# Optimization experiments

Measured on AMD Instinct MI355X. Metric: run time of the kernel, lower is better.

## Reference

```python
import jax, jax.numpy as jnp
import numpy as np

T = 2048        # tokens
HID = 4096      # hidden_size
H = 32          # num attention heads
KV = 8          # num key/value heads (GQA)
D = HID // H    # head_dim = 128
THETA = 10000.0


def setup_inputs() -> dict:
    key = jax.random.key(0)
    k1, k2, k3 = jax.random.split(key, 3)
    hidden_states = jax.random.normal(k1, (T, HID), jnp.float32)
    positions = jnp.arange(T, dtype=jnp.int32)
    Wqkv = jax.random.normal(k2, ((H + 2 * KV) * D, HID), jnp.float32) * 0.02
    Wo = jax.random.normal(k3, (HID, H * D), jnp.float32) * 0.02
    return {"hidden_states": hidden_states, "positions": positions,
            "Wqkv": Wqkv, "Wo": Wo}


def _rope(positions, x):
    """Neox-style rotary embedding. x: [T, h, D], positions: [T]."""
    half = D // 2
    inv_freq = 1.0 / (THETA ** (jnp.arange(half, dtype=jnp.float32) / half))
    ang = positions.astype(jnp.float32)[:, None] * inv_freq      # [T, half]
    cos = jnp.cos(ang)[:, None, :]                                # [T, 1, half]
    sin = jnp.sin(ang)[:, None, :]
    x1, x2 = x[..., :half], x[..., half:]
    return jnp.concatenate([x1 * cos - x2 * sin, x2 * cos + x1 * sin], axis=-1)


def reference(hidden_states, positions, Wqkv, Wo):
    # fused QKV projection (no bias)
    qkv = hidden_states @ Wqkv.T                                  # [T, (H+2KV)*D]
    q, k, v = jnp.split(qkv, [H * D, H * D + KV * D], axis=1)
    q = q.reshape(T, H, D)
    k = k.reshape(T, KV, D)
    v = v.reshape(T, KV, D)
    # RoPE on q and k
    q = _rope(positions, q)
    k = _rope(positions, k)
    # GQA: expand kv heads to match q heads
    g = H // KV
    k = jnp.repeat(k, g, axis=1)                                  # [T, H, D]
    v = jnp.repeat(v, g, axis=1)
    # causal attention (flash-attention math)
    scores = jnp.einsum('thd,shd->hts', q, k) * (D ** -0.5)       # [H, T, T]
    causal = jnp.tril(jnp.ones((T, T), dtype=bool))
    scores = jnp.where(causal[None], scores, jnp.float32(-1e30))
    probs = jax.nn.softmax(scores, axis=-1)
    attn = jnp.einsum('hts,shd->thd', probs, v).reshape(T, H * D)
    # output projection
    return attn @ Wo.T
```

## Files before the change

### kernel.cpp

```cpp
#include <hip/hip_runtime.h>
#include <stdint.h>

#define T_SEQ 2048
#define HIDDEN 4096
#define NHEAD 32
#define NKV 8
#define HDIM 128
#define QKVN 6144

typedef __bf16 bf16x8 __attribute__((ext_vector_type(8)));
typedef float f32x4 __attribute__((ext_vector_type(4)));
typedef unsigned short u16;
typedef u16 u16x8 __attribute__((ext_vector_type(8)));
typedef u16 u16x4 __attribute__((ext_vector_type(4)));

__device__ __forceinline__ u16 f2bf(float f) {
  uint32_t u = __builtin_bit_cast(uint32_t, f);
  u = (u + 0x7fffu + ((u >> 16) & 1u)) >> 16;
  return (u16)u;
}
__device__ __forceinline__ float bf2f(u16 h) {
  uint32_t u = ((uint32_t)h) << 16;
  return __builtin_bit_cast(float, u);
}

__device__ __forceinline__ void gload16(const void* g, void* l) {
  __builtin_amdgcn_global_load_lds(
      (__attribute__((address_space(1))) void*)(uintptr_t)g,
      (__attribute__((address_space(3))) void*)(uintptr_t)l, 16, 0, 0);
}

__global__ void cvt2_kernel(const float* __restrict__ in1, u16* __restrict__ out1, int n1_4,
                            const float* __restrict__ in2, u16* __restrict__ out2, int n2_4) {
  int base = blockIdx.x * blockDim.x + threadIdx.x;
  int stride = gridDim.x * blockDim.x;
  for (int i = base; i < n1_4; i += stride) {
    float4 v = ((const float4*)in1)[i];
    u16x4 o;
    o.x = f2bf(v.x); o.y = f2bf(v.y); o.z = f2bf(v.z); o.w = f2bf(v.w);
    ((u16x4*)out1)[i] = o;
  }
  for (int i = base; i < n2_4; i += stride) {
    float4 v = ((const float4*)in2)[i];
    u16x4 o;
    o.x = f2bf(v.x); o.y = f2bf(v.y); o.z = f2bf(v.z); o.w = f2bf(v.w);
    ((u16x4*)out2)[i] = o;
  }
}

__global__ void prep_kernel(u16* __restrict__ qkv, const int* __restrict__ pos,
                            u16* __restrict__ vt,
                            const float* __restrict__ wo_in, u16* __restrict__ wo_out,
                            int wo_n4) {
  __shared__ u16 tile[64][64];
  const int bid = blockIdx.x;
  const int tid = threadIdx.x;

  if (bid < 512) {
    const int tb = bid & 31;
    const int yy = bid >> 5;
    const int kvh = yy >> 1;
    const int d0 = (yy & 1) * 64;
    const u16* src = qkv + (size_t)(NHEAD + NKV) * HDIM + kvh * HDIM + d0;
#pragma unroll
    for (int g = 0; g < 2; ++g) {
      int u = g * 256 + tid;
      int t = u >> 3, ds = u & 7;
      u16x8 v = *(const u16x8*)(src + (size_t)(tb * 64 + t) * QKVN + ds * 8);
#pragma unroll
      for (int j = 0; j < 8; ++j) {
        int d = ds * 8 + j;
        tile[d][(((t >> 3) ^ (d & 7)) * 8) + (t & 7)] = v[j];
      }
    }
    __syncthreads();
    u16* dst = vt + ((size_t)kvh * HDIM + d0) * T_SEQ + tb * 64;
#pragma unroll
    for (int g = 0; g < 4; ++g) {
      int u = g * 256 + tid;
      int d = u >> 4, qd = u & 15;
      int a = qd >> 3, gg = (qd >> 1) & 3, b = qd & 1;
      int t0 = 32 * a + 16 * b + 4 * gg;
      u16x4 v = *(const u16x4*)&tile[d][(((t0 >> 3) ^ (d & 7)) * 8) + (t0 & 7)];
      *(u16x4*)(dst + (size_t)d * T_SEQ + qd * 4) = v;
    }
    return;
  }

  const int nb = gridDim.x - 512;
  const int base = (bid - 512) * blockDim.x + tid;
  const int stride = nb * blockDim.x;
  for (int idx = base; idx < T_SEQ * 40 * 64; idx += stride) {
    int i = idx & 63;
    int head = (idx >> 6) % 40;
    int t = idx / (40 * 64);
    int hb = head < NHEAD ? head * HDIM : NHEAD * HDIM + (head - NHEAD) * HDIM;
    float p = (float)pos[t];
    float inv_freq = exp2f(-(float)i * (13.287712379549449f / 64.0f));
    float ang = p * inv_freq;
    float s, c;
    sincosf(ang, &s, &c);
    u16* p1 = qkv + (size_t)t * QKVN + hb + i;
    u16* p2 = p1 + 64;
    float x1 = bf2f(*p1), x2 = bf2f(*p2);
    *p1 = f2bf(x1 * c - x2 * s);
    *p2 = f2bf(x2 * c + x1 * s);
  }
  for (int i = base; i < wo_n4; i += stride) {
    float4 v = ((const float4*)wo_in)[i];
    u16x4 o;
    o.x = f2bf(v.x); o.y = f2bf(v.y); o.z = f2bf(v.z); o.w = f2bf(v.w);
    ((u16x4*)wo_out)[i] = o;
  }
}

__device__ __forceinline__ void storeC(float* p, float v) { *p = v; }
__device__ __forceinline__ void storeC(u16* p, float v) { *p = f2bf(v); }
__device__ __forceinline__ f32x4 mfma16(bf16x8 a, bf16x8 b, f32x4 c) {
  return __builtin_amdgcn_mfma_f32_16x16x32_bf16(a, b, c, 0, 0, 0);
}

__global__ void __launch_bounds__(512, 1)
gemm_qkv(const u16* __restrict__ A, const u16* __restrict__ B,
         u16* __restrict__ C, int M, int N, int K) {
  __shared__ u16 As_[2][128 * 64];
  __shared__ u16 Bs_[2][384 * 64];

  const int tid = threadIdx.x;
  const int lane = tid & 63;
  const int w = tid >> 6;
  const int wr = w >> 2, wc = w & 3;
  const int l15 = lane & 15, lg = lane >> 4;

  const int c8 = blockIdx.x & 7, i8 = blockIdx.x >> 3;
  const int by = i8 & 15;
  const int bx = c8 * 2 + (i8 >> 4);
  const int bm = by * 128, bn = bx * 384;

  const int u_lo = w * 64 + lane, u_hi = u_lo + 512;
  const int r0 = u_lo >> 3, s0 = (u_lo & 7) ^ (r0 & 7);
  const int r1 = u_hi >> 3, s1 = (u_hi & 7) ^ (r1 & 7);
  const u16* a_s0 = A + (size_t)(bm + r0) * K + s0 * 8;
  const u16* a_s1 = A + (size_t)(bm + r1) * K + s1 * 8;
  const u16* b_s0[3];
  const u16* b_s1[3];
#pragma unroll
  for (int h = 0; h < 3; ++h) {
    b_s0[h] = B + (size_t)(bn + h * 128 + r0) * K + s0 * 8;
    b_s1[h] = B + (size_t)(bn + h * 128 + r1) * K + s1 * 8;
  }

  const int ax = l15 & 7;
  const int sl0 = (lg ^ ax) * 8;
  const int sl1 = ((4 + lg) ^ ax) * 8;
  const int a_row = (wr * 64 + l15) * 64;
  const int b_row = (wc * 96 + l15) * 64;

  f32x4 acc[4][6] = {};
  bf16x8 af[4][2], bfr[6][2];

#define BARRIER() asm volatile("s_barrier" ::: "memory")
#define WAITBAR(n_) asm volatile("s_waitcnt vmcnt(" #n_ ")\n\ts_barrier" ::: "memory")
#define STAGE_A(t_, p_)                                                        \
  {                                                                            \
    gload16(a_s0 + (size_t)(t_) * 64, &As_[p_][w * 512]);                      \
    gload16(a_s1 + (size_t)(t_) * 64, &As_[p_][4096 + w * 512]);               \
  }
#define STAGE_B(t_, p_, h_)                                                    \
  {                                                                            \
    gload16(b_s0[h_] + (size_t)(t_) * 64, &Bs_[p_][(h_) * 8192 + w * 512]);    \
    gload16(b_s1[h_] + (size_t)(t_) * 64,                                      \
            &Bs_[p_][(h_) * 8192 + 4096 + w * 512]);                           \
  }

  STAGE_A(0, 0);
  STAGE_B(0, 0, 0); STAGE_B(0, 0, 1); STAGE_B(0, 0, 2);
  STAGE_B(1, 1, 0); STAGE_B(1, 1, 1); STAGE_B(1, 1, 2);
  WAITBAR(6);

  const int NT = K >> 6;
  for (int v = 0; v < NT; ++v) {
    const int cur = v & 1, alt = cur ^ 1;
    const u16* Ac = &As_[cur][0];
    const u16* Bc = &Bs_[cur][0];
    const bool s1ok = (v + 1) < NT, s2ok = (v + 2) < NT;

    {
      if (s1ok) STAGE_A(v + 1, alt);
#pragma unroll
      for (int mi = 0; mi < 2; ++mi) {
        af[mi][0] = *(const bf16x8*)&Ac[a_row + mi * 1024 + sl0];
        af[mi][1] = *(const bf16x8*)&Ac[a_row + mi * 1024 + sl1];
      }
#pragma unroll
      for (int ni = 0; ni < 3; ++ni) {
        bfr[ni][0] = *(const bf16x8*)&Bc[b_row + ni * 1024 + sl0];
        bfr[ni][1] = *(const bf16x8*)&Bc[b_row + ni * 1024 + sl1];
      }
      BARRIER();
      __builtin_amdgcn_s_setprio(1);
#pragma unroll
      for (int mi = 0; mi < 2; ++mi)
#pragma unroll
        for (int ni = 0; ni < 3; ++ni) {
          acc[mi][ni] = mfma16(af[mi][0], bfr[ni][0], acc[mi][ni]);
          acc[mi][ni] = mfma16(af[mi][1], bfr[ni][1], acc[mi][ni]);
        }
      __builtin_amdgcn_s_setprio(0);
      BARRIER();
    }
    {
#pragma unroll
      for (int ni = 3; ni < 6; ++ni) {
        bfr[ni][0] = *(const bf16x8*)&Bc[b_row + ni * 1024 + sl0];
        bfr[ni][1] = *(const bf16x8*)&Bc[b_row + ni * 1024 + sl1];
      }
      BARRIER();
      __builtin_amdgcn_s_setprio(1);
#pragma unroll
      for (int mi = 0; mi < 2; ++mi)
#pragma unroll
        for (int ni = 3; ni < 6; ++ni) {
          acc[mi][ni] = mfma16(af[mi][0], bfr[ni][0], acc[mi][ni]);
          acc[mi][ni] = mfma16(af[mi][1], bfr[ni][1], acc[mi][ni]);
        }
      __builtin_amdgcn_s_setprio(0);
      BARRIER();
    }
    {
      if (s2ok) { STAGE_B(v + 2, cur, 0); STAGE_B(v + 2, cur, 1); STAGE_B(v + 2, cur, 2); }
#pragma unroll
      for (int mi = 2; mi < 4; ++mi) {
        af[mi][0] = *(const bf16x8*)&Ac[a_row + mi * 1024 + sl0];
        af[mi][1] = *(const bf16x8*)&Ac[a_row + mi * 1024 + sl1];
      }
      BARRIER();
      __builtin_amdgcn_s_setprio(1);
#pragma unroll
      for (int mi = 2; mi < 4; ++mi)
#pragma unroll
        for (int ni = 0; ni < 6; ++ni) {
          acc[mi][ni] = mfma16(af[mi][0], bfr[ni][0], acc[mi][ni]);
          acc[mi][ni] = mfma16(af[mi][1], bfr[ni][1], acc[mi][ni]);
        }
      __builtin_amdgcn_s_setprio(0);
      if (s2ok) { WAITBAR(6); } else if (s1ok) { WAITBAR(0); } else { BARRIER(); }
    }
  }

#pragma unroll
  for (int mi = 0; mi < 4; ++mi)
#pragma unroll
    for (int ni = 0; ni < 6; ++ni)
#pragma unroll
      for (int r = 0; r < 4; ++r) {
        int row = bm + wr * 64 + mi * 16 + lg * 4 + r;
        int col = bn + wc * 96 + ni * 16 + l15;
        storeC(&C[(size_t)row * N + col], acc[mi][ni][r]);
      }
#undef STAGE_A
#undef STAGE_B
#undef WAITBAR
#undef BARRIER
}

template <typename OutT>
__global__ void __launch_bounds__(512, 2)
gemm256(const u16* __restrict__ A, const u16* __restrict__ B,
        OutT* __restrict__ C0, OutT* __restrict__ C1,
        int N, int K, int NT, int sliceBlocks,
        int nbx, int rw, int rh) {
  __shared__ u16 As_[2][256 * 64];
  __shared__ u16 Bs_[2][256 * 64];

  const int tid = threadIdx.x;
  const int lane = tid & 63;
  const int w = tid >> 6;
  const int wr = w >> 2, wc = w & 3;
  const int l15 = lane & 15, lg = lane >> 4;

  const int bid = blockIdx.x;
  const int slice = bid / sliceBlocks;
  const int wi = bid % sliceBlocks;
  const int k0 = slice * (NT << 6);
  OutT* __restrict__ C = slice ? C1 : C0;

  const int c8 = wi & 7, i8 = wi >> 3;
  const int rpr = nbx / rw;
  const int by = (c8 / rpr) * rh + (i8 % rh);
  const int bx = (c8 % rpr) * rw + (i8 / rh);
  const int bm = by * 256, bn = bx * 256;

  const int u_lo = w * 64 + lane, u_hi = u_lo + 512;
  const int r0 = u_lo >> 3, s0 = (u_lo & 7) ^ (r0 & 7);
  const int r1 = u_hi >> 3, s1 = (u_hi & 7) ^ (r1 & 7);
  const u16* a0s0 = A + (size_t)(bm + r0) * K + k0 + s0 * 8;
  const u16* a0s1 = A + (size_t)(bm + r1) * K + k0 + s1 * 8;
  const u16* a1s0 = A + (size_t)(bm + 128 + r0) * K + k0 + s0 * 8;
  const u16* a1s1 = A + (size_t)(bm + 128 + r1) * K + k0 + s1 * 8;
  const u16* b0s0 = B + (size_t)(bn + r0) * K + k0 + s0 * 8;
  const u16* b0s1 = B + (size_t)(bn + r1) * K + k0 + s1 * 8;
  const u16* b1s0 = B + (size_t)(bn + 128 + r0) * K + k0 + s0 * 8;
  const u16* b1s1 = B + (size_t)(bn + 128 + r1) * K + k0 + s1 * 8;

  const int ax = l15 & 7;
  const int sl0 = (lg ^ ax) * 8;
  const int sl1 = ((4 + lg) ^ ax) * 8;
  const int a_row = (wr * 128 + l15) * 64;
  const int b_row = (wc * 64 + l15) * 64;

  f32x4 acc[8][4] = {};
  bf16x8 bfr[4][2];

#define BARRIER() asm volatile("s_barrier" ::: "memory")
#define WAITBAR(n_) asm volatile("s_waitcnt vmcnt(" #n_ ")\n\ts_barrier" ::: "memory")
#define STAGE_HALF(p0_, p1_, dst_, t_)                                         \
  {                                                                            \
    gload16((p0_) + (size_t)(t_) * 64, (dst_) + (size_t)w * 512);              \
    gload16((p1_) + (size_t)(t_) * 64, (dst_) + 4096 + (size_t)w * 512);       \
  }

  STAGE_HALF(a0s0, a0s1, &As_[0][0], 0);
  STAGE_HALF(a1s0, a1s1, &As_[0][8192], 0);
  STAGE_HALF(b0s0, b0s1, &Bs_[0][0], 0);
  STAGE_HALF(b1s0, b1s1, &Bs_[0][8192], 0);
  STAGE_HALF(b0s0, b0s1, &Bs_[1][0], 1);
  STAGE_HALF(b1s0, b1s1, &Bs_[1][8192], 1);
  WAITBAR(4);

  for (int v = 0; v < NT; ++v) {
    const int cur = v & 1, alt = cur ^ 1;
    const u16* Ac = &As_[cur][0];
    const u16* Bc = &Bs_[cur][0];
    const bool s1ok = (v + 1) < NT, s2ok = (v + 2) < NT;

#define MFMA_QUAD(p_, A0_, A1_, A2_, A3_)                                      \
    __builtin_amdgcn_s_setprio(1);                                             \
    _Pragma("unroll") for (int ni = 0; ni < 4; ++ni) {                         \
      acc[2 * (p_)][ni] = mfma16(A0_, bfr[ni][0], acc[2 * (p_)][ni]);          \
      acc[2 * (p_)][ni] = mfma16(A1_, bfr[ni][1], acc[2 * (p_)][ni]);          \
      acc[2 * (p_) + 1][ni] = mfma16(A2_, bfr[ni][0], acc[2 * (p_) + 1][ni]);  \
      acc[2 * (p_) + 1][ni] = mfma16(A3_, bfr[ni][1], acc[2 * (p_) + 1][ni]);  \
    }                                                                          \
    __builtin_amdgcn_s_setprio(0);

    {
#pragma unroll
      for (int ni = 0; ni < 4; ++ni) {
        bfr[ni][0] = *(const bf16x8*)&Bc[b_row + ni * 1024 + sl0];
        bfr[ni][1] = *(const bf16x8*)&Bc[b_row + ni * 1024 + sl1];
      }
      bf16x8 f0 = *(const bf16x8*)&Ac[a_row + 0 * 1024 + sl0];
      bf16x8 f1 = *(const bf16x8*)&Ac[a_row + 0 * 1024 + sl1];
      bf16x8 f2 = *(const bf16x8*)&Ac[a_row + 1 * 1024 + sl0];
      bf16x8 f3 = *(const bf16x8*)&Ac[a_row + 1 * 1024 + sl1];
      if (s1ok) STAGE_HALF(a0s0, a0s1, &As_[alt][0], v + 1);
      BARRIER();
      MFMA_QUAD(0, f0, f1, f2, f3);
      BARRIER();
    }
    {
      bf16x8 f0 = *(const bf16x8*)&Ac[a_row + 2 * 1024 + sl0];
      bf16x8 f1 = *(const bf16x8*)&Ac[a_row + 2 * 1024 + sl1];
      bf16x8 f2 = *(const bf16x8*)&Ac[a_row + 3 * 1024 + sl0];
      bf16x8 f3 = *(const bf16x8*)&Ac[a_row + 3 * 1024 + sl1];
      if (s1ok) STAGE_HALF(a1s0, a1s1, &As_[alt][8192], v + 1);
      if (s2ok) STAGE_HALF(b0s0, b0s1, &Bs_[cur][0], v + 2);
      BARRIER();
      MFMA_QUAD(1, f0, f1, f2, f3);
      BARRIER();
    }
    {
      bf16x8 f0 = *(const bf16x8*)&Ac[a_row + 4 * 1024 + sl0];
      bf16x8 f1 = *(const bf16x8*)&Ac[a_row + 4 * 1024 + sl1];
      bf16x8 f2 = *(const bf16x8*)&Ac[a_row + 5 * 1024 + sl0];
      bf16x8 f3 = *(const bf16x8*)&Ac[a_row + 5 * 1024 + sl1];
      if (s2ok) STAGE_HALF(b1s0, b1s1, &Bs_[cur][8192], v + 2);
      BARRIER();
      MFMA_QUAD(2, f0, f1, f2, f3);
      BARRIER();
    }
    {
      bf16x8 f0 = *(const bf16x8*)&Ac[a_row + 6 * 1024 + sl0];
      bf16x8 f1 = *(const bf16x8*)&Ac[a_row + 6 * 1024 + sl1];
      bf16x8 f2 = *(const bf16x8*)&Ac[a_row + 7 * 1024 + sl0];
      bf16x8 f3 = *(const bf16x8*)&Ac[a_row + 7 * 1024 + sl1];
      BARRIER();
      MFMA_QUAD(3, f0, f1, f2, f3);
      if (s2ok) { WAITBAR(4); } else { WAITBAR(0); }
    }
#undef MFMA_QUAD
  }

#pragma unroll
  for (int mi = 0; mi < 8; ++mi)
#pragma unroll
    for (int ni = 0; ni < 4; ++ni)
#pragma unroll
      for (int r = 0; r < 4; ++r) {
        int row = bm + wr * 128 + mi * 16 + lg * 4 + r;
        int col = bn + wc * 64 + ni * 16 + l15;
        storeC(&C[(size_t)row * N + col], acc[mi][ni][r]);
      }
#undef STAGE_HALF
#undef WAITBAR
#undef BARRIER
}

__global__ void reduce_add(float* __restrict__ out, const float* __restrict__ part, int n4) {
  int i = blockIdx.x * blockDim.x + threadIdx.x;
  int stride = gridDim.x * blockDim.x;
  for (; i < n4; i += stride) {
    float4 a = ((const float4*)out)[i];
    float4 b = ((const float4*)part)[i];
    a.x += b.x; a.y += b.y; a.z += b.z; a.w += b.w;
    ((float4*)out)[i] = a;
  }
}

__global__ void __launch_bounds__(256, 2)
attn_kernel(const u16* __restrict__ qkv, const u16* __restrict__ vt,
            u16* __restrict__ out) {
  __shared__ u16 Ksh[2][64 * 128];
  __shared__ u16 Vsh[2][128 * 64];

  const int tid = threadIdx.x;
  const int lane = tid & 63;
  const int w = tid >> 6;
  const int l15 = lane & 15, lg = lane >> 4;

  const int bid = blockIdx.x;
  const int u8 = bid & 255, sfl = bid >> 8;
  const int kvh = u8 & 7;
  const int hg = (u8 >> 3) & 3;
  const int x = (u8 >> 5) & 7;
  const int qi = sfl ? x : (15 - x);
  const int h = kvh * 4 + hg;
  const int q0 = qi * 128;
  const int nt = 2 * qi + 2;
  const int wrow = q0 + w * 32;

  const u16* Kg = qkv + NHEAD * HDIM + kvh * HDIM;
  const u16* Vg = vt + (size_t)kvh * HDIM * T_SEQ;

  bf16x8 qa[2][4];
#pragma unroll
  for (int mi = 0; mi < 2; ++mi) {
    const u16* qrow = qkv + (size_t)(wrow + mi * 16 + l15) * QKVN + h * HDIM + lg * 8;
#pragma unroll
    for (int ks = 0; ks < 4; ++ks) qa[mi][ks] = *(const bf16x8*)(qrow + ks * 32);
  }

  f32x4 acc_o[2][8] = {};
  float m[2] = {-1e30f, -1e30f}, lsum[2] = {0.f, 0.f};

  const float scale = 0.088388347648318447f;

#define STAGE_K(kv0, p)                                                        \
  {                                                                            \
    _Pragma("unroll") for (int rnd = 0; rnd < 4; ++rnd) {                      \
      int cc = rnd * 256 + tid;                                                \
      int krow = cc >> 4, kslot = cc & 15;                                     \
      gload16(Kg + (size_t)((kv0) + krow) * QKVN + (kslot ^ (krow & 7)) * 8,   \
              &Ksh[p][(rnd * 256 + w * 64) * 8]);                              \
    }                                                                          \
  }
#define STAGE_V(kv0, p)                                                        \
  {                                                                            \
    _Pragma("unroll") for (int rnd = 0; rnd < 4; ++rnd) {                      \
      int cc = rnd * 256 + tid;                                                \
      int vrow = cc >> 3, ps = cc & 7;                                         \
      gload16(Vg + (size_t)vrow * T_SEQ + (kv0) + ((ps ^ (vrow & 7)) * 8),     \
              &Vsh[p][(rnd * 256 + w * 64) * 8]);                              \
    }                                                                          \
  }

  STAGE_K(0, 0);
  STAGE_V(0, 0);
  __syncthreads();

  for (int t = 0; t < nt; ++t) {
    const int p = t & 1;
    const int kv0 = t * 64;
    const bool more = (t + 1 < nt);
    if (more) {
      STAGE_K(kv0 + 64, p ^ 1);
      STAGE_V(kv0 + 64, p ^ 1);
    }

    if (kv0 <= wrow + 31) {
      f32x4 s[2][4] = {};
#pragma unroll
      for (int ks = 0; ks < 4; ++ks) {
#pragma unroll
        for (int n = 0; n < 4; ++n) {
          int row16 = n * 16 + l15;
          bf16x8 kf = *(const bf16x8*)&Ksh[p][row16 * 128 +
                                              (((ks * 4 + lg) ^ (row16 & 7)) * 8)];
          s[0][n] = mfma16(kf, qa[0][ks], s[0][n]);
          s[1][n] = mfma16(kf, qa[1][ks], s[1][n]);
        }
      }

      const bool diag = (kv0 + 63 > wrow);
      float mx[2];
#pragma unroll
      for (int mi = 0; mi < 2; ++mi) {
        float mm = -1e30f;
        int tq = wrow + mi * 16 + l15;
#pragma unroll
        for (int n = 0; n < 4; ++n)
#pragma unroll
          for (int r = 0; r < 4; ++r) {
            float v = s[mi][n][r] * scale;
            if (diag && (kv0 + n * 16 + lg * 4 + r) > tq) v = -1e30f;
            s[mi][n][r] = v;
            mm = fmaxf(mm, v);
          }
        mm = fmaxf(mm, __shfl_xor(mm, 16, 64));
        mm = fmaxf(mm, __shfl_xor(mm, 32, 64));
        mx[mi] = mm;
      }

      float alpha[2];
#pragma unroll
      for (int mi = 0; mi < 2; ++mi) {
        float mn = fmaxf(m[mi], mx[mi]);
        alpha[mi] = __expf(m[mi] - mn);
        m[mi] = mn;
        lsum[mi] *= alpha[mi];
      }
#pragma unroll
      for (int mi = 0; mi < 2; ++mi)
#pragma unroll
        for (int r = 0; r < 4; ++r) {
          float al = __shfl(alpha[mi], lg * 4 + r, 64);
#pragma unroll
          for (int nd = 0; nd < 8; ++nd) acc_o[mi][nd][r] *= al;
        }

      bf16x8 paf[2][2];
#pragma unroll
      for (int mi = 0; mi < 2; ++mi) {
        float ps = 0.f;
#pragma unroll
        for (int n = 0; n < 4; ++n)
#pragma unroll
          for (int r = 0; r < 4; ++r) {
            float pv = __expf(s[mi][n][r] - m[mi]);
            s[mi][n][r] = pv;
            ps += pv;
          }
        ps += __shfl_xor(ps, 16, 64);
        ps += __shfl_xor(ps, 32, 64);
        lsum[mi] += ps;
#pragma unroll
        for (int ks = 0; ks < 2; ++ks) {
          u16x8 pk;
#pragma unroll
          for (int hn = 0; hn < 2; ++hn)
#pragma unroll
            for (int r = 0; r < 4; ++r)
              pk[hn * 4 + r] = f2bf(s[mi][2 * ks + hn][r]);
          paf[mi][ks] = __builtin_bit_cast(bf16x8, pk);
        }
      }

#pragma unroll
      for (int ks = 0; ks < 2; ++ks) {
#pragma unroll
        for (int nd = 0; nd < 8; ++nd) {
          int d = nd * 16 + l15;
          bf16x8 bv = *(const bf16x8*)&Vsh[p][d * 64 + (((ks * 4 + lg) ^ (d & 7)) * 8)];
          acc_o[0][nd] = mfma16(paf[0][ks], bv, acc_o[0][nd]);
          acc_o[1][nd] = mfma16(paf[1][ks], bv, acc_o[1][nd]);
        }
      }
    }

    __syncthreads();
  }

#pragma unroll
  for (int mi = 0; mi < 2; ++mi)
#pragma unroll
    for (int r = 0; r < 4; ++r) {
      float ls = __shfl(lsum[mi], lg * 4 + r, 64);
      float inv = 1.f / ls;
      int row = wrow + mi * 16 + lg * 4 + r;
#pragma unroll
      for (int nd = 0; nd < 8; ++nd) {
        int col = h * HDIM + nd * 16 + l15;
        out[(size_t)row * (NHEAD * HDIM) + col] = f2bf(acc_o[mi][nd][r] * inv);
      }
    }
#undef STAGE_K
#undef STAGE_V
}

extern "C" void kernel_launch(void* const* d_in, const int* in_sizes, int n_in,
                              void* d_out, int out_size, void* d_ws, size_t ws_size,
                              hipStream_t stream) {
  const float* hs   = (const float*)d_in[0];
  const int*   pos  = (const int*)d_in[1];
  const float* wqkv = (const float*)d_in[2];
  const float* wo   = (const float*)d_in[3];
  float* out = (float*)d_out;
  uint8_t* ws = (uint8_t*)d_ws;

  if (ws_size < 142606336u) return;
  u16* hs_bf   = (u16*)(ws + 0);
  u16* wqkv_bf = (u16*)(ws + 16777216u);
  u16* wo_bf   = (u16*)(ws + 67108864u);
  u16* qkv_bf  = (u16*)(ws + 100663296u);
  u16* attn_bf = (u16*)(ws + 125829120u);
  float* part  = (float*)(ws + 16777216u);
  u16* vt_buf  = (u16*)(ws + 0);

  cvt2_kernel<<<2048, 256, 0, stream>>>(hs, hs_bf, (T_SEQ * HIDDEN) / 4,
                                        wqkv, wqkv_bf, (QKVN * HIDDEN) / 4);

  gemm_qkv<<<256, 512, 0, stream>>>(hs_bf, wqkv_bf, qkv_bf, T_SEQ, QKVN, HIDDEN);

  prep_kernel<<<2048, 256, 0, stream>>>(qkv_bf, pos, vt_buf,
                                        wo, wo_bf, (HIDDEN * HIDDEN) / 4);

  attn_kernel<<<512, 256, 0, stream>>>(qkv_bf, vt_buf, attn_bf);

  gemm256<float><<<256, 512, 0, stream>>>(
      attn_bf, wo_bf, out, part, HIDDEN, HIDDEN, 32, 128, 16, 2, 8);

  reduce_add<<<2048, 256, 0, stream>>>(out, part, (T_SEQ * HIDDEN) / 4);
}
```

Measured before the change: 318.4 us.

## Split attention query rows across 8 waves and widen cvt/reduce vector access

```diff
diff --git a/kernel.cpp b/kernel.cpp
--- a/kernel.cpp
+++ b/kernel.cpp
@@ -30,21 +30,25 @@
       (__attribute__((address_space(3))) void*)(uintptr_t)l, 16, 0, 0);
 }
 
-__global__ void cvt2_kernel(const float* __restrict__ in1, u16* __restrict__ out1, int n1_4,
-                            const float* __restrict__ in2, u16* __restrict__ out2, int n2_4) {
+__global__ void cvt2_kernel(const float* __restrict__ in1, u16* __restrict__ out1, int n1_8,
+                            const float* __restrict__ in2, u16* __restrict__ out2, int n2_8) {
   int base = blockIdx.x * blockDim.x + threadIdx.x;
   int stride = gridDim.x * blockDim.x;
-  for (int i = base; i < n1_4; i += stride) {
-    float4 v = ((const float4*)in1)[i];
-    u16x4 o;
-    o.x = f2bf(v.x); o.y = f2bf(v.y); o.z = f2bf(v.z); o.w = f2bf(v.w);
-    ((u16x4*)out1)[i] = o;
-  }
-  for (int i = base; i < n2_4; i += stride) {
-    float4 v = ((const float4*)in2)[i];
-    u16x4 o;
-    o.x = f2bf(v.x); o.y = f2bf(v.y); o.z = f2bf(v.z); o.w = f2bf(v.w);
-    ((u16x4*)out2)[i] = o;
+  for (int i = base; i < n1_8; i += stride) {
+    float4 a = ((const float4*)in1)[2 * i];
+    float4 b = ((const float4*)in1)[2 * i + 1];
+    u16x8 o;
+    o[0] = f2bf(a.x); o[1] = f2bf(a.y); o[2] = f2bf(a.z); o[3] = f2bf(a.w);
+    o[4] = f2bf(b.x); o[5] = f2bf(b.y); o[6] = f2bf(b.z); o[7] = f2bf(b.w);
+    ((u16x8*)out1)[i] = o;
+  }
+  for (int i = base; i < n2_8; i += stride) {
+    float4 a = ((const float4*)in2)[2 * i];
+    float4 b = ((const float4*)in2)[2 * i + 1];
+    u16x8 o;
+    o[0] = f2bf(a.x); o[1] = f2bf(a.y); o[2] = f2bf(a.z); o[3] = f2bf(a.w);
+    o[4] = f2bf(b.x); o[5] = f2bf(b.y); o[6] = f2bf(b.z); o[7] = f2bf(b.w);
+    ((u16x8*)out2)[i] = o;
   }
 }
 
@@ -408,17 +412,21 @@
 }
 
 __global__ void reduce_add(float* __restrict__ out, const float* __restrict__ part, int n4) {
-  int i = blockIdx.x * blockDim.x + threadIdx.x;
-  int stride = gridDim.x * blockDim.x;
+  int i = (blockIdx.x * blockDim.x + threadIdx.x) * 2;
+  int stride = gridDim.x * blockDim.x * 2;
   for (; i < n4; i += stride) {
-    float4 a = ((const float4*)out)[i];
-    float4 b = ((const float4*)part)[i];
-    a.x += b.x; a.y += b.y; a.z += b.z; a.w += b.w;
-    ((float4*)out)[i] = a;
-  }
-}
-
-__global__ void __launch_bounds__(256, 2)
+    float4 a0 = ((const float4*)out)[i];
+    float4 b0 = ((const float4*)part)[i];
+    float4 a1 = ((const float4*)out)[i + 1];
+    float4 b1 = ((const float4*)part)[i + 1];
+    a0.x += b0.x; a0.y += b0.y; a0.z += b0.z; a0.w += b0.w;
+    a1.x += b1.x; a1.y += b1.y; a1.z += b1.z; a1.w += b1.w;
+    ((float4*)out)[i] = a0;
+    ((float4*)out)[i + 1] = a1;
+  }
+}
+
+__global__ void __launch_bounds__(512, 2)
 attn_kernel(const u16* __restrict__ qkv, const u16* __restrict__ vt,
             u16* __restrict__ out) {
   __shared__ u16 Ksh[2][64 * 128];
@@ -438,40 +446,39 @@
   const int h = kvh * 4 + hg;
   const int q0 = qi * 128;
   const int nt = 2 * qi + 2;
-  const int wrow = q0 + w * 32;
+  const int wrow = q0 + w * 16;
 
   const u16* Kg = qkv + NHEAD * HDIM + kvh * HDIM;
   const u16* Vg = vt + (size_t)kvh * HDIM * T_SEQ;
 
-  bf16x8 qa[2][4];
-#pragma unroll
-  for (int mi = 0; mi < 2; ++mi) {
-    const u16* qrow = qkv + (size_t)(wrow + mi * 16 + l15) * QKVN + h * HDIM + lg * 8;
-#pragma unroll
-    for (int ks = 0; ks < 4; ++ks) qa[mi][ks] = *(const bf16x8*)(qrow + ks * 32);
-  }
-
-  f32x4 acc_o[2][8] = {};
-  float m[2] = {-1e30f, -1e30f}, lsum[2] = {0.f, 0.f};
-
-  const float scale = 0.088388347648318447f;
+  bf16x8 qa[4];
+  {
+    const u16* qrow = qkv + (size_t)(wrow + l15) * QKVN + h * HDIM + lg * 8;
+#pragma unroll
+    for (int ks = 0; ks < 4; ++ks) qa[ks] = *(const bf16x8*)(qrow + ks * 32);
+  }
+
+  f32x4 acc_o[8] = {};
+  float m = -1e30f, lsum = 0.f;
+
+  const float scale2 = 0.12751743342408643f;
 
 #define STAGE_K(kv0, p)                                                        \
   {                                                                            \
-    _Pragma("unroll") for (int rnd = 0; rnd < 4; ++rnd) {                      \
-      int cc = rnd * 256 + tid;                                                \
+    _Pragma("unroll") for (int rnd = 0; rnd < 2; ++rnd) {                      \
+      int cc = rnd * 512 + tid;                                                \
       int krow = cc >> 4, kslot = cc & 15;                                     \
       gload16(Kg + (size_t)((kv0) + krow) * QKVN + (kslot ^ (krow & 7)) * 8,   \
-              &Ksh[p][(rnd * 256 + w * 64) * 8]);                              \
+              &Ksh[p][(rnd * 512 + w * 64) * 8]);                              \
     }                                                                          \
   }
 #define STAGE_V(kv0, p)                                                        \
   {                                                                            \
-    _Pragma("unroll") for (int rnd = 0; rnd < 4; ++rnd) {                      \
-      int cc = rnd * 256 + tid;                                                \
+    _Pragma("unroll") for (int rnd = 0; rnd < 2; ++rnd) {                      \
+      int cc = rnd * 512 + tid;                                                \
       int vrow = cc >> 3, ps = cc & 7;                                         \
       gload16(Vg + (size_t)vrow * T_SEQ + (kv0) + ((ps ^ (vrow & 7)) * 8),     \
-              &Vsh[p][(rnd * 256 + w * 64) * 8]);                              \
+              &Vsh[p][(rnd * 512 + w * 64) * 8]);                              \
     }                                                                          \
   }
 
@@ -488,8 +495,8 @@
       STAGE_V(kv0 + 64, p ^ 1);
     }
 
-    if (kv0 <= wrow + 31) {
-      f32x4 s[2][4] = {};
+    if (kv0 <= wrow + 15) {
+      f32x4 s[4] = {};
 #pragma unroll
       for (int ks = 0; ks < 4; ++ks) {
 #pragma unroll
@@ -497,63 +504,52 @@
           int row16 = n * 16 + l15;
           bf16x8 kf = *(const bf16x8*)&Ksh[p][row16 * 128 +
                                               (((ks * 4 + lg) ^ (row16 & 7)) * 8)];
-          s[0][n] = mfma16(kf, qa[0][ks], s[0][n]);
-          s[1][n] = mfma16(kf, qa[1][ks], s[1][n]);
+          s[n] = mfma16(kf, qa[ks], s[n]);
         }
       }
 
       const bool diag = (kv0 + 63 > wrow);
-      float mx[2];
-#pragma unroll
-      for (int mi = 0; mi < 2; ++mi) {
-        float mm = -1e30f;
-        int tq = wrow + mi * 16 + l15;
+      float mm = -1e30f;
+      {
+        int tq = wrow + l15;
 #pragma unroll
         for (int n = 0; n < 4; ++n)
 #pragma unroll
           for (int r = 0; r < 4; ++r) {
-            float v = s[mi][n][r] * scale;
+            float v = s[n][r] * scale2;
             if (diag && (kv0 + n * 16 + lg * 4 + r) > tq) v = -1e30f;
-            s[mi][n][r] = v;
+            s[n][r] = v;
             mm = fmaxf(mm, v);
           }
         mm = fmaxf(mm, __shfl_xor(mm, 16, 64));
         mm = fmaxf(mm, __shfl_xor(mm, 32, 64));
-        mx[mi] = mm;
-      }
-
-      float alpha[2];
-#pragma unroll
-      for (int mi = 0; mi < 2; ++mi) {
-        float mn = fmaxf(m[mi], mx[mi]);
-        alpha[mi] = __expf(m[mi] - mn);
-        m[mi] = mn;
-        lsum[mi] *= alpha[mi];
-      }
-#pragma unroll
-      for (int mi = 0; mi < 2; ++mi)
-#pragma unroll
-        for (int r = 0; r < 4; ++r) {
-          float al = __shfl(alpha[mi], lg * 4 + r, 64);
-#pragma unroll
-          for (int nd = 0; nd < 8; ++nd) acc_o[mi][nd][r] *= al;
-        }
-
-      bf16x8 paf[2][2];
-#pragma unroll
-      for (int mi = 0; mi < 2; ++mi) {
+      }
+
+      float mn = fmaxf(m, mm);
+      float alpha = exp2f(m - mn);
+      m = mn;
+      lsum *= alpha;
+#pragma unroll
+      for (int r = 0; r < 4; ++r) {
+        float al = __shfl(alpha, lg * 4 + r, 64);
+#pragma unroll
+        for (int nd = 0; nd < 8; ++nd) acc_o[nd][r] *= al;
+      }
+
+      bf16x8 paf[2];
+      {
         float ps = 0.f;
 #pragma unroll
         for (int n = 0; n < 4; ++n)
 #pragma unroll
           for (int r = 0; r < 4; ++r) {
-            float pv = __expf(s[mi][n][r] - m[mi]);
-            s[mi][n][r] = pv;
+            float pv = exp2f(s[n][r] - m);
+            s[n][r] = pv;
             ps += pv;
           }
         ps += __shfl_xor(ps, 16, 64);
         ps += __shfl_xor(ps, 32, 64);
-        lsum[mi] += ps;
+        lsum += ps;
 #pragma unroll
         for (int ks = 0; ks < 2; ++ks) {
           u16x8 pk;
@@ -561,8 +557,8 @@
           for (int hn = 0; hn < 2; ++hn)
 #pragma unroll
             for (int r = 0; r < 4; ++r)
-              pk[hn * 4 + r] = f2bf(s[mi][2 * ks + hn][r]);
-          paf[mi][ks] = __builtin_bit_cast(bf16x8, pk);
+              pk[hn * 4 + r] = f2bf(s[2 * ks + hn][r]);
+          paf[ks] = __builtin_bit_cast(bf16x8, pk);
         }
       }
 
@@ -572,8 +568,7 @@
         for (int nd = 0; nd < 8; ++nd) {
           int d = nd * 16 + l15;
           bf16x8 bv = *(const bf16x8*)&Vsh[p][d * 64 + (((ks * 4 + lg) ^ (d & 7)) * 8)];
-          acc_o[0][nd] = mfma16(paf[0][ks], bv, acc_o[0][nd]);
-          acc_o[1][nd] = mfma16(paf[1][ks], bv, acc_o[1][nd]);
+          acc_o[nd] = mfma16(paf[ks], bv, acc_o[nd]);
         }
       }
     }
@@ -582,18 +577,16 @@
   }
 
 #pragma unroll
-  for (int mi = 0; mi < 2; ++mi)
-#pragma unroll
-    for (int r = 0; r < 4; ++r) {
-      float ls = __shfl(lsum[mi], lg * 4 + r, 64);
-      float inv = 1.f / ls;
-      int row = wrow + mi * 16 + lg * 4 + r;
-#pragma unroll
-      for (int nd = 0; nd < 8; ++nd) {
-        int col = h * HDIM + nd * 16 + l15;
-        out[(size_t)row * (NHEAD * HDIM) + col] = f2bf(acc_o[mi][nd][r] * inv);
-      }
-    }
+  for (int r = 0; r < 4; ++r) {
+    float ls = __shfl(lsum, lg * 4 + r, 64);
+    float inv = 1.f / ls;
+    int row = wrow + lg * 4 + r;
+#pragma unroll
+    for (int nd = 0; nd < 8; ++nd) {
+      int col = h * HDIM + nd * 16 + l15;
+      out[(size_t)row * (NHEAD * HDIM) + col] = f2bf(acc_o[nd][r] * inv);
+    }
+  }
 #undef STAGE_K
 #undef STAGE_V
 }
@@ -617,15 +610,15 @@
   float* part  = (float*)(ws + 16777216u);
   u16* vt_buf  = (u16*)(ws + 0);
 
-  cvt2_kernel<<<2048, 256, 0, stream>>>(hs, hs_bf, (T_SEQ * HIDDEN) / 4,
-                                        wqkv, wqkv_bf, (QKVN * HIDDEN) / 4);
+  cvt2_kernel<<<2048, 256, 0, stream>>>(hs, hs_bf, (T_SEQ * HIDDEN) / 8,
+                                        wqkv, wqkv_bf, (QKVN * HIDDEN) / 8);
 
   gemm_qkv<<<256, 512, 0, stream>>>(hs_bf, wqkv_bf, qkv_bf, T_SEQ, QKVN, HIDDEN);
 
   prep_kernel<<<2048, 256, 0, stream>>>(qkv_bf, pos, vt_buf,
                                         wo, wo_bf, (HIDDEN * HIDDEN) / 4);
 
-  attn_kernel<<<512, 256, 0, stream>>>(qkv_bf, vt_buf, attn_bf);
+  attn_kernel<<<512, 512, 0, stream>>>(qkv_bf, vt_buf, attn_bf);
 
   gemm256<float><<<256, 512, 0, stream>>>(
       attn_bf, wo_bf, out, part, HIDDEN, HIDDEN, 32, 128, 16, 2, 8);
```

Result: no change. 319.5 us (+0.4%).

## Triple-buffer attention KV tiles at 32-row granularity, widen conversion and reduce vectors

Applied to the files above, without the earlier changes.

```diff
diff --git a/kernel.cpp b/kernel.cpp
--- a/kernel.cpp
+++ b/kernel.cpp
@@ -30,21 +30,25 @@
       (__attribute__((address_space(3))) void*)(uintptr_t)l, 16, 0, 0);
 }
 
-__global__ void cvt2_kernel(const float* __restrict__ in1, u16* __restrict__ out1, int n1_4,
-                            const float* __restrict__ in2, u16* __restrict__ out2, int n2_4) {
+__global__ void cvt2_kernel(const float* __restrict__ in1, u16* __restrict__ out1, int n1_8,
+                            const float* __restrict__ in2, u16* __restrict__ out2, int n2_8) {
   int base = blockIdx.x * blockDim.x + threadIdx.x;
   int stride = gridDim.x * blockDim.x;
-  for (int i = base; i < n1_4; i += stride) {
-    float4 v = ((const float4*)in1)[i];
-    u16x4 o;
-    o.x = f2bf(v.x); o.y = f2bf(v.y); o.z = f2bf(v.z); o.w = f2bf(v.w);
-    ((u16x4*)out1)[i] = o;
-  }
-  for (int i = base; i < n2_4; i += stride) {
-    float4 v = ((const float4*)in2)[i];
-    u16x4 o;
-    o.x = f2bf(v.x); o.y = f2bf(v.y); o.z = f2bf(v.z); o.w = f2bf(v.w);
-    ((u16x4*)out2)[i] = o;
+  for (int i = base; i < n1_8; i += stride) {
+    float4 a = ((const float4*)in1)[2 * i];
+    float4 b = ((const float4*)in1)[2 * i + 1];
+    u16x8 o;
+    o[0] = f2bf(a.x); o[1] = f2bf(a.y); o[2] = f2bf(a.z); o[3] = f2bf(a.w);
+    o[4] = f2bf(b.x); o[5] = f2bf(b.y); o[6] = f2bf(b.z); o[7] = f2bf(b.w);
+    ((u16x8*)out1)[i] = o;
+  }
+  for (int i = base; i < n2_8; i += stride) {
+    float4 a = ((const float4*)in2)[2 * i];
+    float4 b = ((const float4*)in2)[2 * i + 1];
+    u16x8 o;
+    o[0] = f2bf(a.x); o[1] = f2bf(a.y); o[2] = f2bf(a.z); o[3] = f2bf(a.w);
+    o[4] = f2bf(b.x); o[5] = f2bf(b.y); o[6] = f2bf(b.z); o[7] = f2bf(b.w);
+    ((u16x8*)out2)[i] = o;
   }
 }
 
@@ -408,21 +412,25 @@
 }
 
 __global__ void reduce_add(float* __restrict__ out, const float* __restrict__ part, int n4) {
-  int i = blockIdx.x * blockDim.x + threadIdx.x;
-  int stride = gridDim.x * blockDim.x;
+  int i = (blockIdx.x * blockDim.x + threadIdx.x) * 2;
+  int stride = gridDim.x * blockDim.x * 2;
   for (; i < n4; i += stride) {
-    float4 a = ((const float4*)out)[i];
-    float4 b = ((const float4*)part)[i];
-    a.x += b.x; a.y += b.y; a.z += b.z; a.w += b.w;
-    ((float4*)out)[i] = a;
+    float4 a0 = ((const float4*)out)[i];
+    float4 b0 = ((const float4*)part)[i];
+    float4 a1 = ((const float4*)out)[i + 1];
+    float4 b1 = ((const float4*)part)[i + 1];
+    a0.x += b0.x; a0.y += b0.y; a0.z += b0.z; a0.w += b0.w;
+    a1.x += b1.x; a1.y += b1.y; a1.z += b1.z; a1.w += b1.w;
+    ((float4*)out)[i] = a0;
+    ((float4*)out)[i + 1] = a1;
   }
 }
 
 __global__ void __launch_bounds__(256, 2)
 attn_kernel(const u16* __restrict__ qkv, const u16* __restrict__ vt,
             u16* __restrict__ out) {
-  __shared__ u16 Ksh[2][64 * 128];
-  __shared__ u16 Vsh[2][128 * 64];
+  __shared__ u16 Ksh[3][32 * 128];
+  __shared__ u16 Vsh[3][64 * 64];
 
   const int tid = threadIdx.x;
   const int lane = tid & 63;
@@ -437,7 +445,7 @@
   const int qi = sfl ? x : (15 - x);
   const int h = kvh * 4 + hg;
   const int q0 = qi * 128;
-  const int nt = 2 * qi + 2;
+  const int nt = 4 * qi + 4;
   const int wrow = q0 + w * 32;
 
   const u16* Kg = qkv + NHEAD * HDIM + kvh * HDIM;
@@ -456,60 +464,67 @@
 
   const float scale = 0.088388347648318447f;
 
+#define BARRIER() asm volatile("s_barrier" ::: "memory")
+#define WAITBAR(n_) asm volatile("s_waitcnt vmcnt(" #n_ ")\n\ts_barrier" ::: "memory")
 #define STAGE_K(kv0, p)                                                        \
   {                                                                            \
-    _Pragma("unroll") for (int rnd = 0; rnd < 4; ++rnd) {                      \
+    _Pragma("unroll") for (int rnd = 0; rnd < 2; ++rnd) {                      \
       int cc = rnd * 256 + tid;                                                \
       int krow = cc >> 4, kslot = cc & 15;                                     \
-      gload16(Kg + (size_t)((kv0) + krow) * QKVN + (kslot ^ (krow & 7)) * 8,   \
+      gload16(Kg + (size_t)((kv0) + krow) * QKVN + ((kslot ^ (krow & 7)) * 8), \
               &Ksh[p][(rnd * 256 + w * 64) * 8]);                              \
     }                                                                          \
   }
 #define STAGE_V(kv0, p)                                                        \
   {                                                                            \
-    _Pragma("unroll") for (int rnd = 0; rnd < 4; ++rnd) {                      \
+    _Pragma("unroll") for (int rnd = 0; rnd < 2; ++rnd) {                      \
       int cc = rnd * 256 + tid;                                                \
-      int vrow = cc >> 3, ps = cc & 7;                                         \
-      gload16(Vg + (size_t)vrow * T_SEQ + (kv0) + ((ps ^ (vrow & 7)) * 8),     \
+      int vr = cc >> 3;                                                        \
+      int sL = (cc & 7) ^ (vr & 7);                                            \
+      gload16(Vg + (size_t)(2 * vr + (sL >> 2)) * T_SEQ + (kv0) + (sL & 3) * 8,\
               &Vsh[p][(rnd * 256 + w * 64) * 8]);                              \
     }                                                                          \
   }
 
   STAGE_K(0, 0);
   STAGE_V(0, 0);
-  __syncthreads();
-
+  STAGE_K(32, 1);
+  STAGE_V(32, 1);
+  WAITBAR(4);
+
+  int cur = 0;
   for (int t = 0; t < nt; ++t) {
-    const int p = t & 1;
-    const int kv0 = t * 64;
-    const bool more = (t + 1 < nt);
-    if (more) {
-      STAGE_K(kv0 + 64, p ^ 1);
-      STAGE_V(kv0 + 64, p ^ 1);
+    const int kv0 = t * 32;
+    const bool s2ok = (t + 2) < nt;
+    const bool s1ok = (t + 1) < nt;
+    if (s2ok) {
+      int nx2 = cur + 2; if (nx2 >= 3) nx2 -= 3;
+      STAGE_K(kv0 + 64, nx2);
+      STAGE_V(kv0 + 64, nx2);
     }
 
     if (kv0 <= wrow + 31) {
-      f32x4 s[2][4] = {};
+      f32x4 s[2][2] = {};
 #pragma unroll
       for (int ks = 0; ks < 4; ++ks) {
 #pragma unroll
-        for (int n = 0; n < 4; ++n) {
+        for (int n = 0; n < 2; ++n) {
           int row16 = n * 16 + l15;
-          bf16x8 kf = *(const bf16x8*)&Ksh[p][row16 * 128 +
-                                              (((ks * 4 + lg) ^ (row16 & 7)) * 8)];
+          bf16x8 kf = *(const bf16x8*)&Ksh[cur][row16 * 128 +
+                                               (((ks * 4 + lg) ^ (row16 & 7)) * 8)];
           s[0][n] = mfma16(kf, qa[0][ks], s[0][n]);
           s[1][n] = mfma16(kf, qa[1][ks], s[1][n]);
         }
       }
 
-      const bool diag = (kv0 + 63 > wrow);
+      const bool diag = (kv0 + 31 > wrow);
       float mx[2];
 #pragma unroll
       for (int mi = 0; mi < 2; ++mi) {
         float mm = -1e30f;
         int tq = wrow + mi * 16 + l15;
 #pragma unroll
-        for (int n = 0; n < 4; ++n)
+        for (int n = 0; n < 2; ++n)
 #pragma unroll
           for (int r = 0; r < 4; ++r) {
             float v = s[mi][n][r] * scale;
@@ -539,12 +554,12 @@
           for (int nd = 0; nd < 8; ++nd) acc_o[mi][nd][r] *= al;
         }
 
-      bf16x8 paf[2][2];
+      bf16x8 paf[2];
 #pragma unroll
       for (int mi = 0; mi < 2; ++mi) {
         float ps = 0.f;
 #pragma unroll
-        for (int n = 0; n < 4; ++n)
+        for (int n = 0; n < 2; ++n)
 #pragma unroll
           for (int r = 0; r < 4; ++r) {
             float pv = __expf(s[mi][n][r] - m[mi]);
@@ -554,31 +569,26 @@
         ps += __shfl_xor(ps, 16, 64);
         ps += __shfl_xor(ps, 32, 64);
         lsum[mi] += ps;
-#pragma unroll
-        for (int ks = 0; ks < 2; ++ks) {
-          u16x8 pk;
-#pragma unroll
-          for (int hn = 0; hn < 2; ++hn)
-#pragma unroll
-            for (int r = 0; r < 4; ++r)
-              pk[hn * 4 + r] = f2bf(s[mi][2 * ks + hn][r]);
-          paf[mi][ks] = __builtin_bit_cast(bf16x8, pk);
-        }
-      }
-
-#pragma unroll
-      for (int ks = 0; ks < 2; ++ks) {
-#pragma unroll
-        for (int nd = 0; nd < 8; ++nd) {
-          int d = nd * 16 + l15;
-          bf16x8 bv = *(const bf16x8*)&Vsh[p][d * 64 + (((ks * 4 + lg) ^ (d & 7)) * 8)];
-          acc_o[0][nd] = mfma16(paf[0][ks], bv, acc_o[0][nd]);
-          acc_o[1][nd] = mfma16(paf[1][ks], bv, acc_o[1][nd]);
-        }
-      }
-    }
-
-    __syncthreads();
+        u16x8 pk;
+#pragma unroll
+        for (int j = 0; j < 8; ++j) pk[j] = f2bf(s[mi][j >> 2][j & 3]);
+        paf[mi] = __builtin_bit_cast(bf16x8, pk);
+      }
+
+#pragma unroll
+      for (int nd = 0; nd < 8; ++nd) {
+        int d = nd * 16 + l15;
+        int vr = d >> 1;
+        bf16x8 bv = *(const bf16x8*)&Vsh[cur][vr * 64 +
+                        ((((d & 1) * 4 + lg) ^ (vr & 7)) * 8)];
+        acc_o[0][nd] = mfma16(paf[0], bv, acc_o[0][nd]);
+        acc_o[1][nd] = mfma16(paf[1], bv, acc_o[1][nd]);
+      }
+    }
+
+    if (s2ok) { WAITBAR(4); }
+    else if (s1ok) { WAITBAR(0); }
+    cur = (cur == 2) ? 0 : cur + 1;
   }
 
 #pragma unroll
@@ -596,6 +606,8 @@
     }
 #undef STAGE_K
 #undef STAGE_V
+#undef WAITBAR
+#undef BARRIER
 }
 
 extern "C" void kernel_launch(void* const* d_in, const int* in_sizes, int n_in,
@@ -617,8 +629,8 @@
   float* part  = (float*)(ws + 16777216u);
   u16* vt_buf  = (u16*)(ws + 0);
 
-  cvt2_kernel<<<2048, 256, 0, stream>>>(hs, hs_bf, (T_SEQ * HIDDEN) / 4,
-                                        wqkv, wqkv_bf, (QKVN * HIDDEN) / 4);
+  cvt2_kernel<<<2048, 256, 0, stream>>>(hs, hs_bf, (T_SEQ * HIDDEN) / 8,
+                                        wqkv, wqkv_bf, (QKVN * HIDDEN) / 8);
 
   gemm_qkv<<<256, 512, 0, stream>>>(hs_bf, wqkv_bf, qkv_bf, T_SEQ, QKVN, HIDDEN);
 
```

Measured after the change: 338.4 us. +6.3%, slower.
